# Optimization experiments

Measured on AMD Instinct MI355X. Metric: run time of the kernel, lower is better.

The kernel has to match this reference:

```python
import jax, jax.numpy as jnp
import numpy as np

B, S, H, NH = 1, 4096, 768, 12
D = H // NH  # per-head dim = 64


def setup_inputs() -> dict:
    key = jax.random.key(0)
    ks = jax.random.split(key, 10)
    p = 0.02  # param scale
    return {
        "x": jax.random.normal(ks[0], (B, S, H), jnp.float32),
        "Wq": jax.random.normal(ks[1], (H, H), jnp.float32) * p,
        "bq": jax.random.normal(ks[2], (H,), jnp.float32) * p,
        "Wk": jax.random.normal(ks[3], (H, H), jnp.float32) * p,
        "bk": jax.random.normal(ks[4], (H,), jnp.float32) * p,
        "Wv": jax.random.normal(ks[5], (H, H), jnp.float32) * p,
        "bv": jax.random.normal(ks[6], (H,), jnp.float32) * p,
        "Wo": jax.random.normal(ks[7], (H, H), jnp.float32) * p,
        "bo": jax.random.normal(ks[8], (H,), jnp.float32) * p,
        "attn_mask": jax.random.randint(ks[9], (B, 1, 1, S), 0, 2).astype(bool),
    }


def _split_heads(t):
    # [B, S, H] -> [B, NH, S, D]
    return t.reshape(B, S, NH, D).transpose(0, 2, 1, 3)


def reference(x, Wq, bq, Wk, bk, Wv, bv, Wo, bo, attn_mask):
    q = _split_heads(x @ Wq.T + bq)
    k = _split_heads(x @ Wk.T + bk)
    v = _split_heads(x @ Wv.T + bv)
    scores = jnp.einsum('bhqd,bhkd->bhqk', q, k) / np.sqrt(D).astype(np.float32)
    scores = jnp.where(attn_mask, jnp.float32(-1e9), scores)
    attn = jax.nn.softmax(scores, axis=-1)
    ctx = jnp.einsum('bhqk,bhkd->bhqd', attn, v)
    ctx = ctx.transpose(0, 2, 1, 3).reshape(B, S, H)  # merge heads
    return ctx @ Wo.T + bo
```

## Files before the change

kernel.cpp:

```cpp
#include <hip/hip_runtime.h>
#include <stdint.h>

#define S_LEN 4096
#define HDIM  768
#define NHEAD 12
#define DHEAD 64

typedef _Float16 f16;
typedef __attribute__((ext_vector_type(8)))  _Float16 f16x8;
typedef __attribute__((ext_vector_type(4)))  _Float16 f16x4;
typedef __attribute__((ext_vector_type(4)))  float    f32x4;
typedef __attribute__((ext_vector_type(16))) float    f32x16;

typedef __attribute__((address_space(1))) void gv_t;
typedef __attribute__((address_space(3))) void lv_t;

__device__ __forceinline__ void async_copy16(const void* g, void* l) {
  __builtin_amdgcn_global_load_lds((gv_t*)g, (lv_t*)l, 16, 0, 0);
}

__device__ __forceinline__ float fast_exp2(float x) {
#if __has_builtin(__builtin_amdgcn_exp2f)
  return __builtin_amdgcn_exp2f(x);
#else
  return exp2f(x);
#endif
}

__device__ __forceinline__ int swz4(int row) { return (row ^ (row >> 2)) & 3; }

constexpr size_t OFF_META = 0;
constexpr size_t OFF_RIDX = 256;
constexpr size_t OFF_XB   = 65536;
constexpr size_t SZ_XB    = (size_t)S_LEN * HDIM * 2;
constexpr size_t OFF_WQKV = OFF_XB + SZ_XB;
constexpr size_t SZ_WQKV  = (size_t)3 * HDIM * HDIM * 2;
constexpr size_t OFF_WO   = OFF_WQKV + SZ_WQKV;
constexpr size_t SZ_WO    = (size_t)HDIM * HDIM * 2;
constexpr size_t OFF_Q    = OFF_WO + SZ_WO;
constexpr size_t SZ_HD    = (size_t)NHEAD * S_LEN * DHEAD * 2;
constexpr size_t OFF_K    = OFF_Q + SZ_HD;
constexpr size_t OFF_VT   = OFF_K + SZ_HD;
constexpr size_t OFF_VR   = OFF_VT + SZ_HD;
constexpr size_t OFF_PO1  = OFF_VR + SZ_HD;

__global__ __launch_bounds__(256) void k_prep(const float* __restrict__ x,
                                              const float* __restrict__ wq,
                                              const float* __restrict__ wk,
                                              const float* __restrict__ wv,
                                              const float* __restrict__ wo,
                                              const int* __restrict__ mi,
                                              f16* __restrict__ dst,
                                              int* __restrict__ ridx,
                                              int* __restrict__ meta) {
  __shared__ int s_flag;
  __shared__ int s_cnt[256];
  const int b = blockIdx.x, tid = threadIdx.x;
  if (b < 5376) {
    int i = b * 256 + tid;
    const float* src; int off;
    if (i < 786432) { src = x; off = i; }
    else {
      int j = i - 786432;
      int w = j / 147456;
      off = j - w * 147456;
      src = (w == 0) ? wq : (w == 1) ? wk : (w == 2) ? wv : wo;
    }
    float4 v = ((const float4*)src)[off];
    f16x4 h;
    h[0] = (f16)v.x; h[1] = (f16)v.y; h[2] = (f16)v.z; h[3] = (f16)v.w;
    ((f16x4*)dst)[i] = h;
    return;
  }
  if (tid == 0) s_flag = 1;
  __syncthreads();
  int bad = 0;
  #pragma unroll
  for (int k = 0; k < 4; ++k) {
    int v = mi[k * 256 + tid];
    if (v != 0 && v != 1) bad = 1;
  }
  if (bad) atomicAnd(&s_flag, 0);
  __syncthreads();
  const int isInt = s_flag;
  const unsigned char* mu8 = (const unsigned char*)mi;
  int keep[16]; int cnt = 0;
  const int s0 = tid * 16;
  #pragma unroll
  for (int k = 0; k < 16; ++k) {
    int mval = isInt ? mi[s0 + k] : (int)mu8[s0 + k];
    keep[k] = (mval == 0) ? 1 : 0;
    cnt += keep[k];
    ridx[s0 + k] = 0;
  }
  s_cnt[tid] = cnt;
  __syncthreads();
  for (int off = 1; off < 256; off <<= 1) {
    int t = (tid >= off) ? s_cnt[tid - off] : 0;
    __syncthreads();
    s_cnt[tid] += t;
    __syncthreads();
  }
  int base = s_cnt[tid] - cnt;
  #pragma unroll
  for (int k = 0; k < 16; ++k) {
    if (keep[k]) { ridx[base] = s0 + k; ++base; }
  }
  if (tid == 255) meta[0] = s_cnt[255];
}

__global__ __launch_bounds__(256) void k_qkv(
    const f16* __restrict__ xb, const f16* __restrict__ wqkv,
    const float* __restrict__ bq, const float* __restrict__ bk, const float* __restrict__ bv,
    const int* __restrict__ ridx, const int* __restrict__ meta,
    f16* __restrict__ Qh, f16* __restrict__ Kc, f16* __restrict__ Vrow) {
  __shared__ __attribute__((aligned(16))) f16 lA[128 * 32];
  __shared__ __attribute__((aligned(16))) f16 lB[128 * 32];
  const int tid = threadIdx.x;
  const int wid = tid >> 6, lane = tid & 63;
  const int hf = lane >> 5, l31 = lane & 31;
  const int wm = wid >> 1, wn = wid & 1;
  const int tn = blockIdx.x;
  const int m0 = blockIdx.y * 128;
  const int mat = tn / 6;
  const int nb = (tn % 6) * 128;
  const int kc = meta[0];
  if (mat != 0 && m0 >= kc) return;
  const f16* wbase = wqkv + (size_t)mat * HDIM * HDIM;

  const int ar0 = tid >> 2, ar1 = 64 + (tid >> 2);
  const f16* asrc0;
  const f16* asrc1;
  if (mat == 0) {
    asrc0 = xb + (size_t)(m0 + ar0) * HDIM;
    asrc1 = xb + (size_t)(m0 + ar1) * HDIM;
  } else {
    int g0 = (m0 + ar0 < kc) ? ridx[m0 + ar0] : 0;
    int g1 = (m0 + ar1 < kc) ? ridx[m0 + ar1] : 0;
    asrc0 = xb + (size_t)g0 * HDIM;
    asrc1 = xb + (size_t)g1 * HDIM;
  }
  const int slot = tid & 3;
  const int gs0 = slot ^ swz4(ar0);
  const int gs1 = slot ^ swz4(ar1);

  f32x16 acc[2][2] = {};

  for (int k0 = 0; k0 < HDIM; k0 += 32) {
    async_copy16((const char*)(asrc0 + k0) + gs0 * 16, (char*)lA + (wid * 64) * 16);
    async_copy16((const char*)(asrc1 + k0) + gs1 * 16, (char*)lA + (256 + wid * 64) * 16);
    async_copy16((const char*)(wbase + (size_t)(nb + ar0) * HDIM + k0) + gs0 * 16,
                 (char*)lB + (wid * 64) * 16);
    async_copy16((const char*)(wbase + (size_t)(nb + ar1) * HDIM + k0) + gs1 * 16,
                 (char*)lB + (256 + wid * 64) * 16);
    __syncthreads();
    #pragma unroll
    for (int kk = 0; kk < 2; ++kk) {
      f16x8 af[2], bf[2];
      #pragma unroll
      for (int mi = 0; mi < 2; ++mi) {
        int row = wm * 64 + mi * 32 + l31;
        af[mi] = *(const f16x8*)&lA[row * 32 + (((kk * 2 + hf) ^ swz4(row)) * 8)];
      }
      #pragma unroll
      for (int ni = 0; ni < 2; ++ni) {
        int row = wn * 64 + ni * 32 + l31;
        bf[ni] = *(const f16x8*)&lB[row * 32 + (((kk * 2 + hf) ^ swz4(row)) * 8)];
      }
      #pragma unroll
      for (int mi = 0; mi < 2; ++mi)
        #pragma unroll
        for (int ni = 0; ni < 2; ++ni)
          acc[mi][ni] = __builtin_amdgcn_mfma_f32_32x32x16_f16(af[mi], bf[ni], acc[mi][ni], 0, 0, 0);
    }
    __syncthreads();
  }

  const float* bias = (mat == 0) ? bq : (mat == 1) ? bk : bv;
  const float qscale = 0.125f * 1.44269504088896341f;
  f16* kvdst = (mat == 1) ? Kc : Vrow;
  #pragma unroll
  for (int mi = 0; mi < 2; ++mi) {
    #pragma unroll
    for (int ni = 0; ni < 2; ++ni) {
      int n = nb + wn * 64 + ni * 32 + l31;
      int head = n >> 6, d = n & 63;
      float b = bias[n];
      #pragma unroll
      for (int reg = 0; reg < 16; ++reg) {
        int s = m0 + wm * 64 + mi * 32 + (reg & 3) + 8 * (reg >> 2) + 4 * hf;
        float val = acc[mi][ni][reg] + b;
        if (mat == 0) {
          Qh[((size_t)head * S_LEN + s) * DHEAD + d] = (f16)(val * qscale);
        } else if (s < kc) {
          kvdst[((size_t)head * S_LEN + s) * DHEAD + d] = (f16)val;
        }
      }
    }
  }
}

__global__ __launch_bounds__(256) void k_vt(const int* __restrict__ meta,
                                            const f16* __restrict__ Vrow,
                                            f16* __restrict__ Vtc,
                                            f16* __restrict__ Kc) {
  const int kc = meta[0];
  const int kcp = (kc + 63) & ~63;
  const int p0 = blockIdx.x * 64;
  const int h = blockIdx.y;
  const int tid = threadIdx.x;
  if (p0 >= kcp) return;
  if (p0 <= kc && kc < p0 + 64 && kc < kcp) {
    const int npad = kcp - kc;
    for (int u = tid; u < npad * 8; u += 256) {
      int r = kc + (u >> 3), c8 = u & 7;
      f16x8 z = {};
      *(f16x8*)&Kc[((size_t)h * S_LEN + r) * DHEAD + c8 * 8] = z;
    }
  }
  __shared__ __attribute__((aligned(16))) f16 lT[64 * 80];
  for (int u = tid; u < 512; u += 256) {
    int d8 = u >> 6, p = u & 63;
    f16x8 v = {};
    if (p0 + p < kc) v = *(const f16x8*)&Vrow[((size_t)h * S_LEN + p0 + p) * DHEAD + d8 * 8];
    #pragma unroll
    for (int j = 0; j < 8; ++j) lT[(d8 * 8 + j) * 80 + p] = v[j];
  }
  __syncthreads();
  for (int w = tid; w < 512; w += 256) {
    int d = w >> 3, p8 = w & 7;
    int base16 = (p8 >> 1) * 16, half = p8 & 1;
    f16x4 lo = *(const f16x4*)&lT[d * 80 + base16 + half * 4];
    f16x4 hi = *(const f16x4*)&lT[d * 80 + base16 + 8 + half * 4];
    f16x8 o;
    o[0] = lo[0]; o[1] = lo[1]; o[2] = lo[2]; o[3] = lo[3];
    o[4] = hi[0]; o[5] = hi[1]; o[6] = hi[2]; o[7] = hi[3];
    *(f16x8*)&Vtc[((size_t)h * DHEAD + d) * S_LEN + p0 + p8 * 8] = o;
  }
}

__global__ __launch_bounds__(256, 3) void k_attn(
    const f16* __restrict__ Qh, const f16* __restrict__ Kc, const f16* __restrict__ Vtc,
    const int* __restrict__ meta, f16* __restrict__ PO0, f16* __restrict__ PO1,
    float* __restrict__ PL) {
  __shared__ __attribute__((aligned(16))) f16 lK[2][64 * 64];
  __shared__ __attribute__((aligned(16))) f16 lV[2][64 * 64];
  const int tid = threadIdx.x;
  const int wid = tid >> 6, lane = tid & 63;
  const int hf = lane >> 5, l31 = lane & 31, r7 = l31 & 7;

  const int lid = blockIdx.x;
  const int w = ((lid & 7) * 96) + (lid >> 3);
  const int head = w >> 6;
  const int rem = w & 63;
  const int split = rem >> 5;
  const int q0 = (rem & 31) * 128 + wid * 32;

  const int kc = meta[0];
  const int nkt = (kc + 63) >> 6;
  const int th = nkt >> 1;
  const int t0 = split ? th : 0;
  const int t1 = split ? nkt : th;

  const f16* Qp = Qh + ((size_t)head * S_LEN + q0 + l31) * DHEAD;
  f16x8 qf[4];
  #pragma unroll
  for (int dc = 0; dc < 4; ++dc) qf[dc] = *(const f16x8*)(Qp + dc * 16 + hf * 8);

  f32x16 accO[2] = {};
  float ls0 = 0.f, ls1 = 0.f, ls2 = 0.f, ls3 = 0.f;

  const char* kbase = (const char*)(Kc + (size_t)head * S_LEN * DHEAD);
  const char* vbase = (const char*)(Vtc + (size_t)head * DHEAD * S_LEN);

  const int c0row = tid >> 3,        c0slot = tid & 7;
  const int c1row = (256 + tid) >> 3, c1slot = tid & 7;
  const int gs0 = c0slot ^ (c0row & 7);
  const int gs1 = c1slot ^ (c1row & 7);

  auto stage = [&](int t, int buf) {
    const int j0 = t * 64;
    async_copy16(kbase + (size_t)(j0 + c0row) * 128 + gs0 * 16,
                 (char*)&lK[buf][0] + (wid * 64) * 16);
    async_copy16(vbase + (size_t)c0row * (S_LEN * 2) + (size_t)j0 * 2 + gs0 * 16,
                 (char*)&lV[buf][0] + (wid * 64) * 16);
    async_copy16(kbase + (size_t)(j0 + c1row) * 128 + gs1 * 16,
                 (char*)&lK[buf][0] + (256 + wid * 64) * 16);
    async_copy16(vbase + (size_t)c1row * (S_LEN * 2) + (size_t)j0 * 2 + gs1 * 16,
                 (char*)&lV[buf][0] + (256 + wid * 64) * 16);
  };

  int cur = 0;
  if (t0 < t1) {
    stage(t0, 0);
    __syncthreads();
  }

  for (int t = t0; t < t1; ++t) {
    const bool more = (t + 1 < t1);
    if (more) stage(t + 1, cur ^ 1);

    #pragma unroll
    for (int mh = 0; mh < 2; ++mh) {
      f16x8 af[4];
      const int arow = mh * 32 + l31;
      #pragma unroll
      for (int dc = 0; dc < 4; ++dc)
        af[dc] = *(const f16x8*)&lK[cur][arow * 64 + ((((dc << 1) | hf) ^ r7) * 8)];
      f32x16 s = {};
      #pragma unroll
      for (int dc = 0; dc < 4; ++dc)
        s = __builtin_amdgcn_mfma_f32_32x32x16_f16(af[dc], qf[dc], s, 0, 0, 0);
      #pragma unroll
      for (int u = 0; u < 16; ++u) {
        s[u] = fast_exp2(s[u]);
        if ((u & 3) == 0) ls0 += s[u];
        else if ((u & 3) == 1) ls1 += s[u];
        else if ((u & 3) == 2) ls2 += s[u];
        else ls3 += s[u];
      }
      #pragma unroll
      for (int cc = 0; cc < 2; ++cc) {
        f16x8 pf;
        #pragma unroll
        for (int u = 0; u < 8; ++u) pf[u] = (f16)s[8 * cc + u];
        const int c2 = mh * 2 + cc;
        #pragma unroll
        for (int dh = 0; dh < 2; ++dh) {
          const int vrow = dh * 32 + l31;
          f16x8 vf = *(const f16x8*)&lV[cur][vrow * 64 + ((((c2 << 1) | hf) ^ r7) * 8)];
          accO[dh] = __builtin_amdgcn_mfma_f32_32x32x16_f16(pf, vf, accO[dh], 0, 0, 0);
        }
      }
    }

    if (more) {
      __syncthreads();
      cur ^= 1;
    }
  }

  float lsum = (ls0 + ls1) + (ls2 + ls3);
  lsum += __shfl_xor(lsum, 32);
  if (split == 1) lsum -= (float)(nkt * 64 - kc);
  if (hf == 0)
    PL[((size_t)split * NHEAD + head) * S_LEN + q0 + l31] = lsum;

  f16* PO = split ? PO1 : PO0;
  #pragma unroll
  for (int dh = 0; dh < 2; ++dh)
    #pragma unroll
    for (int reg = 0; reg < 16; ++reg) {
      int row = (reg & 3) + 8 * (reg >> 2) + 4 * hf;
      PO[((size_t)head * S_LEN + q0 + row) * DHEAD + dh * 32 + l31] = (f16)accO[dh][reg];
    }
}

__global__ __launch_bounds__(256) void k_out(
    const f16* __restrict__ PO0, const f16* __restrict__ PO1,
    const float* __restrict__ PL, const f16* __restrict__ wo,
    const float* __restrict__ bo, float* __restrict__ out) {
  __shared__ __attribute__((aligned(16))) f16 lA[128 * 32];
  __shared__ __attribute__((aligned(16))) f16 lB[128 * 32];
  __shared__ float linv[NHEAD * 128];
  const int tid = threadIdx.x;
  const int wid = tid >> 6, lane = tid & 63;
  const int hf = lane >> 5, l31 = lane & 31;
  const int wm = wid >> 1, wn = wid & 1;
  const int nb = blockIdx.x * 128;
  const int m0 = blockIdx.y * 128;

  for (int i = tid; i < NHEAD * 128; i += 256) {
    int h = i >> 7, r = i & 127;
    float l = PL[(size_t)h * S_LEN + m0 + r] + PL[(size_t)(NHEAD + h) * S_LEN + m0 + r];
    linv[i] = 1.0f / l;
  }
  __syncthreads();

  f32x16 acc[2][2] = {};

  for (int k0 = 0; k0 < HDIM; k0 += 32) {
    const int head = k0 >> 6, d0 = k0 & 63;
    #pragma unroll
    for (int iss = 0; iss < 2; ++iss) {
      int c = iss * 256 + tid;
      int row = c >> 2, slot = c & 3;
      int gs = slot ^ swz4(row);
      size_t pi = ((size_t)head * S_LEN + m0 + row) * DHEAD + d0 + gs * 8;
      f16x8 a0 = *(const f16x8*)(PO0 + pi);
      f16x8 a1 = *(const f16x8*)(PO1 + pi);
      float il = linv[head * 128 + row];
      f16x8 av;
      #pragma unroll
      for (int u = 0; u < 8; ++u) av[u] = (f16)(((float)a0[u] + (float)a1[u]) * il);
      *(f16x8*)&lA[c * 8] = av;
      async_copy16((const char*)(wo + (size_t)(nb + row) * HDIM + k0) + gs * 16,
                   (char*)lB + (iss * 256 + wid * 64) * 16);
    }
    __syncthreads();
    #pragma unroll
    for (int kk = 0; kk < 2; ++kk) {
      f16x8 af[2], bf[2];
      #pragma unroll
      for (int mi = 0; mi < 2; ++mi) {
        int row = wm * 64 + mi * 32 + l31;
        af[mi] = *(const f16x8*)&lA[row * 32 + (((kk * 2 + hf) ^ swz4(row)) * 8)];
      }
      #pragma unroll
      for (int ni = 0; ni < 2; ++ni) {
        int row = wn * 64 + ni * 32 + l31;
        bf[ni] = *(const f16x8*)&lB[row * 32 + (((kk * 2 + hf) ^ swz4(row)) * 8)];
      }
      #pragma unroll
      for (int mi = 0; mi < 2; ++mi)
        #pragma unroll
        for (int ni = 0; ni < 2; ++ni)
          acc[mi][ni] = __builtin_amdgcn_mfma_f32_32x32x16_f16(af[mi], bf[ni], acc[mi][ni], 0, 0, 0);
    }
    __syncthreads();
  }

  #pragma unroll
  for (int mi = 0; mi < 2; ++mi) {
    #pragma unroll
    for (int ni = 0; ni < 2; ++ni) {
      int n = nb + wn * 64 + ni * 32 + l31;
      float b = bo[n];
      #pragma unroll
      for (int reg = 0; reg < 16; ++reg) {
        int s = m0 + wm * 64 + mi * 32 + (reg & 3) + 8 * (reg >> 2) + 4 * hf;
        out[(size_t)s * HDIM + n] = acc[mi][ni][reg] + b;
      }
    }
  }
}

extern "C" void kernel_launch(void* const* d_in, const int* in_sizes, int n_in,
                              void* d_out, int out_size, void* d_ws, size_t ws_size,
                              hipStream_t stream) {
  const float* x  = (const float*)d_in[0];
  const float* Wq = (const float*)d_in[1];
  const float* bq = (const float*)d_in[2];
  const float* Wk = (const float*)d_in[3];
  const float* bk = (const float*)d_in[4];
  const float* Wv = (const float*)d_in[5];
  const float* bv = (const float*)d_in[6];
  const float* Wo = (const float*)d_in[7];
  const float* bo = (const float*)d_in[8];
  const int*   mask = (const int*)d_in[9];
  float* out = (float*)d_out;

  char* ws = (char*)d_ws;
  int* meta  = (int*)(ws + OFF_META);
  int* ridx  = (int*)(ws + OFF_RIDX);
  f16* xb    = (f16*)(ws + OFF_XB);
  f16* wqkv  = (f16*)(ws + OFF_WQKV);
  f16* wob   = (f16*)(ws + OFF_WO);
  f16* Qh    = (f16*)(ws + OFF_Q);
  f16* Kc    = (f16*)(ws + OFF_K);
  f16* Vtc   = (f16*)(ws + OFF_VT);
  f16* Vrow  = (f16*)(ws + OFF_VR);
  f16* PO0   = (f16*)(ws + OFF_VR);
  f16* PO1   = (f16*)(ws + OFF_PO1);
  float* PL  = (float*)(ws + OFF_WQKV);

  k_prep<<<dim3(5377), 256, 0, stream>>>(x, Wq, Wk, Wv, Wo, mask, xb, ridx, meta);
  k_qkv<<<dim3(18, 32), 256, 0, stream>>>(xb, wqkv, bq, bk, bv, ridx, meta, Qh, Kc, Vrow);
  k_vt<<<dim3(64, NHEAD), 256, 0, stream>>>(meta, Vrow, Vtc, Kc);
  k_attn<<<dim3(768), 256, 0, stream>>>(Qh, Kc, Vtc, meta, PO0, PO1, PL);
  k_out<<<dim3(6, 32), 256, 0, stream>>>(PO0, PO1, PL, wob, bo, out);
}
```

Measured before the change: 178.2 us.

## Double-buffer QKV and output GEMMs, split attention into four KV chunks

The QKV projection and output projection GEMMs now use double-buffered LDS tiles, so loads for the next K-slice overlap MFMA work on the current one. The attention kernel now handles 64 query rows per wave (two 32-row blocks), which reuses each K/V fragment twice. It also splits the KV range into four parts instead of two and writes four partial outputs and row sums. The output kernel combines the four partials when it stages the A tile. The cost is more register pressure in attention, extra partial-output memory traffic, and larger LDS use.

Result: slower. 219.1 us (+22.9%).

```diff
diff --git a/kernel.cpp b/kernel.cpp
--- a/kernel.cpp
+++ b/kernel.cpp
@@ -43,6 +43,8 @@
 constexpr size_t OFF_VT   = OFF_K + SZ_HD;
 constexpr size_t OFF_VR   = OFF_VT + SZ_HD;
 constexpr size_t OFF_PO1  = OFF_VR + SZ_HD;
+constexpr size_t OFF_PO2  = OFF_PO1 + SZ_HD;
+constexpr size_t OFF_PO3  = OFF_PO2 + SZ_HD;
 
 __global__ __launch_bounds__(256) void k_prep(const float* __restrict__ x,
                                               const float* __restrict__ wq,
@@ -114,8 +116,8 @@
     const float* __restrict__ bq, const float* __restrict__ bk, const float* __restrict__ bv,
     const int* __restrict__ ridx, const int* __restrict__ meta,
     f16* __restrict__ Qh, f16* __restrict__ Kc, f16* __restrict__ Vrow) {
-  __shared__ __attribute__((aligned(16))) f16 lA[128 * 32];
-  __shared__ __attribute__((aligned(16))) f16 lB[128 * 32];
+  __shared__ __attribute__((aligned(16))) f16 lA[2][128 * 32];
+  __shared__ __attribute__((aligned(16))) f16 lB[2][128 * 32];
   const int tid = threadIdx.x;
   const int wid = tid >> 6, lane = tid & 63;
   const int hf = lane >> 5, l31 = lane & 31;
@@ -144,28 +146,36 @@
   const int gs0 = slot ^ swz4(ar0);
   const int gs1 = slot ^ swz4(ar1);
 
+  auto stage = [&](int k0, int buf) {
+    async_copy16((const char*)(asrc0 + k0) + gs0 * 16, (char*)&lA[buf][0] + (wid * 64) * 16);
+    async_copy16((const char*)(asrc1 + k0) + gs1 * 16, (char*)&lA[buf][0] + (256 + wid * 64) * 16);
+    async_copy16((const char*)(wbase + (size_t)(nb + ar0) * HDIM + k0) + gs0 * 16,
+                 (char*)&lB[buf][0] + (wid * 64) * 16);
+    async_copy16((const char*)(wbase + (size_t)(nb + ar1) * HDIM + k0) + gs1 * 16,
+                 (char*)&lB[buf][0] + (256 + wid * 64) * 16);
+  };
+
   f32x16 acc[2][2] = {};
 
+  stage(0, 0);
+  __syncthreads();
+  int cur = 0;
+
   for (int k0 = 0; k0 < HDIM; k0 += 32) {
-    async_copy16((const char*)(asrc0 + k0) + gs0 * 16, (char*)lA + (wid * 64) * 16);
-    async_copy16((const char*)(asrc1 + k0) + gs1 * 16, (char*)lA + (256 + wid * 64) * 16);
-    async_copy16((const char*)(wbase + (size_t)(nb + ar0) * HDIM + k0) + gs0 * 16,
-                 (char*)lB + (wid * 64) * 16);
-    async_copy16((const char*)(wbase + (size_t)(nb + ar1) * HDIM + k0) + gs1 * 16,
-                 (char*)lB + (256 + wid * 64) * 16);
-    __syncthreads();
+    const bool more = (k0 + 32 < HDIM);
+    if (more) stage(k0 + 32, cur ^ 1);
     #pragma unroll
     for (int kk = 0; kk < 2; ++kk) {
       f16x8 af[2], bf[2];
       #pragma unroll
       for (int mi = 0; mi < 2; ++mi) {
         int row = wm * 64 + mi * 32 + l31;
-        af[mi] = *(const f16x8*)&lA[row * 32 + (((kk * 2 + hf) ^ swz4(row)) * 8)];
+        af[mi] = *(const f16x8*)&lA[cur][row * 32 + (((kk * 2 + hf) ^ swz4(row)) * 8)];
       }
       #pragma unroll
       for (int ni = 0; ni < 2; ++ni) {
         int row = wn * 64 + ni * 32 + l31;
-        bf[ni] = *(const f16x8*)&lB[row * 32 + (((kk * 2 + hf) ^ swz4(row)) * 8)];
+        bf[ni] = *(const f16x8*)&lB[cur][row * 32 + (((kk * 2 + hf) ^ swz4(row)) * 8)];
       }
       #pragma unroll
       for (int mi = 0; mi < 2; ++mi)
@@ -173,7 +183,7 @@
         for (int ni = 0; ni < 2; ++ni)
           acc[mi][ni] = __builtin_amdgcn_mfma_f32_32x32x16_f16(af[mi], bf[ni], acc[mi][ni], 0, 0, 0);
     }
-    __syncthreads();
+    if (more) { __syncthreads(); cur ^= 1; }
   }
 
   const float* bias = (mat == 0) ? bq : (mat == 1) ? bk : bv;
@@ -241,7 +251,9 @@
 
 __global__ __launch_bounds__(256, 3) void k_attn(
     const f16* __restrict__ Qh, const f16* __restrict__ Kc, const f16* __restrict__ Vtc,
-    const int* __restrict__ meta, f16* __restrict__ PO0, f16* __restrict__ PO1,
+    const int* __restrict__ meta,
+    f16* __restrict__ PO0, f16* __restrict__ PO1,
+    f16* __restrict__ PO2, f16* __restrict__ PO3,
     float* __restrict__ PL) {
   __shared__ __attribute__((aligned(16))) f16 lK[2][64 * 64];
   __shared__ __attribute__((aligned(16))) f16 lV[2][64 * 64];
@@ -253,27 +265,29 @@
   const int w = ((lid & 7) * 96) + (lid >> 3);
   const int head = w >> 6;
   const int rem = w & 63;
-  const int split = rem >> 5;
-  const int q0 = (rem & 31) * 128 + wid * 32;
+  const int split = rem >> 4;
+  const int qw = (rem & 15) * 256 + wid * 64;
 
   const int kc = meta[0];
   const int nkt = (kc + 63) >> 6;
-  const int th = nkt >> 1;
-  const int t0 = split ? th : 0;
-  const int t1 = split ? nkt : th;
-
-  const f16* Qp = Qh + ((size_t)head * S_LEN + q0 + l31) * DHEAD;
-  f16x8 qf[4];
-  #pragma unroll
-  for (int dc = 0; dc < 4; ++dc) qf[dc] = *(const f16x8*)(Qp + dc * 16 + hf * 8);
-
-  f32x16 accO[2] = {};
-  float ls0 = 0.f, ls1 = 0.f, ls2 = 0.f, ls3 = 0.f;
+  const int t0 = (split * nkt) >> 2;
+  const int t1 = ((split + 1) * nkt) >> 2;
+
+  f16x8 qf[2][4];
+  #pragma unroll
+  for (int qb = 0; qb < 2; ++qb) {
+    const f16* Qp = Qh + ((size_t)head * S_LEN + qw + qb * 32 + l31) * DHEAD;
+    #pragma unroll
+    for (int dc = 0; dc < 4; ++dc) qf[qb][dc] = *(const f16x8*)(Qp + dc * 16 + hf * 8);
+  }
+
+  f32x16 accO[2][2] = {};
+  float ls[2][2] = {};
 
   const char* kbase = (const char*)(Kc + (size_t)head * S_LEN * DHEAD);
   const char* vbase = (const char*)(Vtc + (size_t)head * DHEAD * S_LEN);
 
-  const int c0row = tid >> 3,        c0slot = tid & 7;
+  const int c0row = tid >> 3,         c0slot = tid & 7;
   const int c1row = (256 + tid) >> 3, c1slot = tid & 7;
   const int gs0 = c0slot ^ (c0row & 7);
   const int gs1 = c1slot ^ (c1row & 7);
@@ -307,29 +321,33 @@
       #pragma unroll
       for (int dc = 0; dc < 4; ++dc)
         af[dc] = *(const f16x8*)&lK[cur][arow * 64 + ((((dc << 1) | hf) ^ r7) * 8)];
-      f32x16 s = {};
-      #pragma unroll
-      for (int dc = 0; dc < 4; ++dc)
-        s = __builtin_amdgcn_mfma_f32_32x32x16_f16(af[dc], qf[dc], s, 0, 0, 0);
-      #pragma unroll
-      for (int u = 0; u < 16; ++u) {
-        s[u] = fast_exp2(s[u]);
-        if ((u & 3) == 0) ls0 += s[u];
-        else if ((u & 3) == 1) ls1 += s[u];
-        else if ((u & 3) == 2) ls2 += s[u];
-        else ls3 += s[u];
+
+      f16x8 pf[2][2];
+      #pragma unroll
+      for (int qb = 0; qb < 2; ++qb) {
+        f32x16 s = {};
+        #pragma unroll
+        for (int dc = 0; dc < 4; ++dc)
+          s = __builtin_amdgcn_mfma_f32_32x32x16_f16(af[dc], qf[qb][dc], s, 0, 0, 0);
+        #pragma unroll
+        for (int u = 0; u < 16; ++u) {
+          s[u] = fast_exp2(s[u]);
+          ls[qb][u & 1] += s[u];
+        }
+        #pragma unroll
+        for (int cc = 0; cc < 2; ++cc)
+          #pragma unroll
+          for (int u = 0; u < 8; ++u) pf[qb][cc][u] = (f16)s[8 * cc + u];
       }
       #pragma unroll
       for (int cc = 0; cc < 2; ++cc) {
-        f16x8 pf;
-        #pragma unroll
-        for (int u = 0; u < 8; ++u) pf[u] = (f16)s[8 * cc + u];
         const int c2 = mh * 2 + cc;
         #pragma unroll
         for (int dh = 0; dh < 2; ++dh) {
           const int vrow = dh * 32 + l31;
           f16x8 vf = *(const f16x8*)&lV[cur][vrow * 64 + ((((c2 << 1) | hf) ^ r7) * 8)];
-          accO[dh] = __builtin_amdgcn_mfma_f32_32x32x16_f16(pf, vf, accO[dh], 0, 0, 0);
+          accO[0][dh] = __builtin_amdgcn_mfma_f32_32x32x16_f16(pf[0][cc], vf, accO[0][dh], 0, 0, 0);
+          accO[1][dh] = __builtin_amdgcn_mfma_f32_32x32x16_f16(pf[1][cc], vf, accO[1][dh], 0, 0, 0);
         }
       }
     }
@@ -340,28 +358,32 @@
     }
   }
 
-  float lsum = (ls0 + ls1) + (ls2 + ls3);
-  lsum += __shfl_xor(lsum, 32);
-  if (split == 1) lsum -= (float)(nkt * 64 - kc);
-  if (hf == 0)
-    PL[((size_t)split * NHEAD + head) * S_LEN + q0 + l31] = lsum;
-
-  f16* PO = split ? PO1 : PO0;
-  #pragma unroll
-  for (int dh = 0; dh < 2; ++dh)
-    #pragma unroll
-    for (int reg = 0; reg < 16; ++reg) {
-      int row = (reg & 3) + 8 * (reg >> 2) + 4 * hf;
-      PO[((size_t)head * S_LEN + q0 + row) * DHEAD + dh * 32 + l31] = (f16)accO[dh][reg];
-    }
+  f16* PO = (split == 0) ? PO0 : (split == 1) ? PO1 : (split == 2) ? PO2 : PO3;
+  #pragma unroll
+  for (int qb = 0; qb < 2; ++qb) {
+    float lsum = ls[qb][0] + ls[qb][1];
+    lsum += __shfl_xor(lsum, 32);
+    if (t1 == nkt) lsum -= (float)(nkt * 64 - kc);
+    if (hf == 0)
+      PL[((size_t)split * NHEAD + head) * S_LEN + qw + qb * 32 + l31] = lsum;
+    #pragma unroll
+    for (int dh = 0; dh < 2; ++dh)
+      #pragma unroll
+      for (int reg = 0; reg < 16; ++reg) {
+        int row = (reg & 3) + 8 * (reg >> 2) + 4 * hf;
+        PO[((size_t)head * S_LEN + qw + qb * 32 + row) * DHEAD + dh * 32 + l31] =
+            (f16)accO[qb][dh][reg];
+      }
+  }
 }
 
 __global__ __launch_bounds__(256) void k_out(
     const f16* __restrict__ PO0, const f16* __restrict__ PO1,
+    const f16* __restrict__ PO2, const f16* __restrict__ PO3,
     const float* __restrict__ PL, const f16* __restrict__ wo,
     const float* __restrict__ bo, float* __restrict__ out) {
-  __shared__ __attribute__((aligned(16))) f16 lA[128 * 32];
-  __shared__ __attribute__((aligned(16))) f16 lB[128 * 32];
+  __shared__ __attribute__((aligned(16))) f16 lA[2][128 * 32];
+  __shared__ __attribute__((aligned(16))) f16 lB[2][128 * 32];
   __shared__ float linv[NHEAD * 128];
   const int tid = threadIdx.x;
   const int wid = tid >> 6, lane = tid & 63;
@@ -372,44 +394,78 @@
 
   for (int i = tid; i < NHEAD * 128; i += 256) {
     int h = i >> 7, r = i & 127;
-    float l = PL[(size_t)h * S_LEN + m0 + r] + PL[(size_t)(NHEAD + h) * S_LEN + m0 + r];
+    float l = PL[(size_t)h * S_LEN + m0 + r]
+            + PL[(size_t)(NHEAD + h) * S_LEN + m0 + r]
+            + PL[(size_t)(2 * NHEAD + h) * S_LEN + m0 + r]
+            + PL[(size_t)(3 * NHEAD + h) * S_LEN + m0 + r];
     linv[i] = 1.0f / l;
   }
   __syncthreads();
 
-  f32x16 acc[2][2] = {};
-
-  for (int k0 = 0; k0 < HDIM; k0 += 32) {
+  const int row0 = tid >> 2, row1 = 64 + (tid >> 2);
+  const int slot = tid & 3;
+  const int gsa0 = slot ^ swz4(row0);
+  const int gsa1 = slot ^ swz4(row1);
+  const float il0 = linv[0];
+
+  f16x8 areg[2][4];
+  auto loadA = [&](int k0) {
     const int head = k0 >> 6, d0 = k0 & 63;
+    size_t pi0 = ((size_t)head * S_LEN + m0 + row0) * DHEAD + d0 + gsa0 * 8;
+    size_t pi1 = ((size_t)head * S_LEN + m0 + row1) * DHEAD + d0 + gsa1 * 8;
+    areg[0][0] = *(const f16x8*)(PO0 + pi0);
+    areg[0][1] = *(const f16x8*)(PO1 + pi0);
+    areg[0][2] = *(const f16x8*)(PO2 + pi0);
+    areg[0][3] = *(const f16x8*)(PO3 + pi0);
+    areg[1][0] = *(const f16x8*)(PO0 + pi1);
+    areg[1][1] = *(const f16x8*)(PO1 + pi1);
+    areg[1][2] = *(const f16x8*)(PO2 + pi1);
+    areg[1][3] = *(const f16x8*)(PO3 + pi1);
+  };
+  auto commitA = [&](int k0, int buf) {
+    const int head = k0 >> 6;
     #pragma unroll
     for (int iss = 0; iss < 2; ++iss) {
-      int c = iss * 256 + tid;
-      int row = c >> 2, slot = c & 3;
-      int gs = slot ^ swz4(row);
-      size_t pi = ((size_t)head * S_LEN + m0 + row) * DHEAD + d0 + gs * 8;
-      f16x8 a0 = *(const f16x8*)(PO0 + pi);
-      f16x8 a1 = *(const f16x8*)(PO1 + pi);
+      int row = iss ? row1 : row0;
       float il = linv[head * 128 + row];
       f16x8 av;
       #pragma unroll
-      for (int u = 0; u < 8; ++u) av[u] = (f16)(((float)a0[u] + (float)a1[u]) * il);
-      *(f16x8*)&lA[c * 8] = av;
-      async_copy16((const char*)(wo + (size_t)(nb + row) * HDIM + k0) + gs * 16,
-                   (char*)lB + (iss * 256 + wid * 64) * 16);
-    }
-    __syncthreads();
+      for (int u = 0; u < 8; ++u)
+        av[u] = (f16)((((float)areg[iss][0][u] + (float)areg[iss][1][u]) +
+                       ((float)areg[iss][2][u] + (float)areg[iss][3][u])) * il);
+      *(f16x8*)&lA[buf][(iss * 256 + tid) * 8] = av;
+    }
+  };
+  auto stageB = [&](int k0, int buf) {
+    async_copy16((const char*)(wo + (size_t)(nb + row0) * HDIM + k0) + gsa0 * 16,
+                 (char*)&lB[buf][0] + (wid * 64) * 16);
+    async_copy16((const char*)(wo + (size_t)(nb + row1) * HDIM + k0) + gsa1 * 16,
+                 (char*)&lB[buf][0] + (256 + wid * 64) * 16);
+  };
+
+  f32x16 acc[2][2] = {};
+
+  loadA(0);
+  stageB(0, 0);
+  commitA(0, 0);
+  __syncthreads();
+  int cur = 0;
+
+  for (int k0 = 0; k0 < HDIM; k0 += 32) {
+    const bool more = (k0 + 32 < HDIM);
+    if (more) { loadA(k0 + 32); stageB(k0 + 32, cur ^ 1); }
     #pragma unroll
     for (int kk = 0; kk < 2; ++kk) {
       f16x8 af[2], bf[2];
       #pragma unroll
       for (int mi = 0; mi < 2; ++mi) {
         int row = wm * 64 + mi * 32 + l31;
-        af[mi] = *(const f16x8*)&lA[row * 32 + (((kk * 2 + hf) ^ swz4(row)) * 8)];
+        af[mi] = *(const f16x8*)&lA[cur][row * 32 + (((kk * 2 + hf) ^ swz4(row)) * 8)];
       }
       #pragma unroll
       for (int ni = 0; ni < 2; ++ni) {
         int row = wn * 64 + ni * 32 + l31;
-        bf[ni] = *(const f16x8*)&lB[row * 32 + (((kk * 2 + hf) ^ swz4(row)) * 8)];
+        bf[ni] = *(const f16x8*)&lB[cur][row * 32 + (((kk * 2 + hf) ^ swz4(row)) * 8)];
       }
       #pragma unroll
       for (int mi = 0; mi < 2; ++mi)
@@ -417,7 +473,11 @@
         for (int ni = 0; ni < 2; ++ni)
           acc[mi][ni] = __builtin_amdgcn_mfma_f32_32x32x16_f16(af[mi], bf[ni], acc[mi][ni], 0, 0, 0);
     }
-    __syncthreads();
+    if (more) {
+      commitA(k0 + 32, cur ^ 1);
+      __syncthreads();
+      cur ^= 1;
+    }
   }
 
   #pragma unroll
@@ -462,11 +522,13 @@
   f16* Vrow  = (f16*)(ws + OFF_VR);
   f16* PO0   = (f16*)(ws + OFF_VR);
   f16* PO1   = (f16*)(ws + OFF_PO1);
+  f16* PO2   = (f16*)(ws + OFF_PO2);
+  f16* PO3   = (f16*)(ws + OFF_PO3);
   float* PL  = (float*)(ws + OFF_WQKV);
 
   k_prep<<<dim3(5377), 256, 0, stream>>>(x, Wq, Wk, Wv, Wo, mask, xb, ridx, meta);
   k_qkv<<<dim3(18, 32), 256, 0, stream>>>(xb, wqkv, bq, bk, bv, ridx, meta, Qh, Kc, Vrow);
   k_vt<<<dim3(64, NHEAD), 256, 0, stream>>>(meta, Vrow, Vtc, Kc);
-  k_attn<<<dim3(768), 256, 0, stream>>>(Qh, Kc, Vtc, meta, PO0, PO1, PL);
-  k_out<<<dim3(6, 32), 256, 0, stream>>>(PO0, PO1, PL, wob, bo, out);
-}
+  k_attn<<<dim3(768), 256, 0, stream>>>(Qh, Kc, Vtc, meta, PO0, PO1, PO2, PO3, PL);
+  k_out<<<dim3(6, 32), 256, 0, stream>>>(PO0, PO1, PO2, PO3, PL, wob, bo, out);
+}
```
